# Performance work log

Hardware: AMD Instinct MI355X
Metric: run time of the kernel (lower is better)

Reference implementation:

```python
import jax, jax.numpy as jnp
import numpy as np

B, C_IN, H, W = 1, 448, 64, 64   # concat of resnet18 layer1/2/3 resized to 64x64: 64+128+256=448
D, L = 100, 4096                 # projection dim, number of spatial locations (gaussian params)
OUT_HW = 256                     # input_size for final bilinear upsample


def setup_inputs() -> dict:
    key = jax.random.key(0)
    k0, k1, k2, k3, k4 = jax.random.split(key, 5)
    return {
        "features": jax.random.normal(k0, (B, C_IN, H, W), jnp.float32),
        "proj_w": jax.random.normal(k1, (D, C_IN), jnp.float32) * 0.05,
        "proj_b": jax.random.normal(k2, (D,), jnp.float32) * 0.05,
        "mean": jax.random.normal(k3, (D, L), jnp.float32),
        "inv_cov": jax.random.normal(k4, (L, D, D), jnp.float32) * 0.01,
    }


def reference(features, proj_w, proj_b, mean, inv_cov):
    Bn, C, Hh, Ww = features.shape
    # permute(0,2,3,1).reshape(-1, C) then Linear(C, D)
    f = features.transpose(0, 2, 3, 1).reshape(-1, C)          # (N, C), N = B*H*W
    f = f @ proj_w.T + proj_b                                  # (N, D)
    m = mean.T                                                 # (L, D)
    # Batched Mahalanobis-style quadratic form replacing the Python loop over L=4096:
    #   dist[n, l] = (f_n - m_l)^T  inv_cov_l  (f_n - m_l)
    # Expanded so the heavy term is a single (N, D*D) x (D*D, L) GEMM (no (N,L,D) intermediate).
    Cm  = jnp.einsum('lde,le->ld', inv_cov, m)                 # inv_cov_l @ m_l        (L, D)
    CTm = jnp.einsum('lde,ld->le', inv_cov, m)                 # inv_cov_l^T @ m_l      (L, D)
    const = jnp.einsum('ld,ld->l', m, Cm)                      # m_l^T inv_cov_l m_l    (L,)
    ff = (f[:, :, None] * f[:, None, :]).reshape(f.shape[0], D * D)   # outer(f,f) flattened (N, D*D)
    quad = ff @ inv_cov.reshape(L, D * D).T                    # f^T inv_cov_l f        (N, L)
    dist = quad - f @ (Cm + CTm).T + const[None, :]            # (N, L)
    min_d = jnp.min(dist, axis=1).reshape(Bn, Hh, Ww)[:, None, :, :]  # (B, 1, H, W)
    amap = (min_d - min_d.min()) / (min_d.max() - min_d.min() + 1e-8)
    amap = jax.image.resize(amap, (Bn, 1, OUT_HW, OUT_HW), method='bilinear')
    return amap
```

## Files before the change

kernel.cpp:

```cpp
#include <hip/hip_runtime.h>
#include <hip/hip_bf16.h>
#include <stdint.h>

#define CIN   448
#define DP    100
#define NPIX  4096
#define LNUM  4096
#define KQ    5050
#define KLIN  5150
#define KTOT  5184
#define KSTEPS (KTOT / 64)
#define OUTHW 256

typedef _Float16 f16_t;
typedef _Float16 f16x8 __attribute__((ext_vector_type(8)));
typedef float    f32x4 __attribute__((ext_vector_type(4)));

static __device__ __forceinline__ int swz_idx(int r, int kin) {
    return r * 64 + ((kin & 56) ^ ((r & 7) << 3)) + (kin & 7);
}

static __device__ __forceinline__ int tri_off(int d) { return (d * (201 - d)) >> 1; }

static __device__ __forceinline__ void unpack_tri(int k, int& d, int& e) {
    int dd = (int)((201.0f - sqrtf(40401.0f - 8.0f * (float)k)) * 0.5f);
    if (dd < 0) dd = 0;
    if (dd > 99) dd = 99;
    while (tri_off(dd + 1) <= k) ++dd;
    while (tri_off(dd) > k) --dd;
    d = dd;
    e = dd + (k - tri_off(dd));
}

static __device__ __forceinline__ unsigned f2u(float x) {
    unsigned b = __float_as_uint(x);
    return (b & 0x80000000u) ? ~b : (b | 0x80000000u);
}
static __device__ __forceinline__ float u2f(unsigned u) {
    unsigned b = (u & 0x80000000u) ? (u & 0x7FFFFFFFu) : ~u;
    return __uint_as_float(b);
}

static __device__ __forceinline__ void gload_lds16(const f16_t* g, f16_t* l) {
    __builtin_amdgcn_global_load_lds((const __attribute__((address_space(1))) unsigned*)g,
                                     (__attribute__((address_space(3))) unsigned*)l,
                                     16, 0, 0);
}

__global__ void k_proj(const float* __restrict__ feat, const float* __restrict__ w,
                       const float* __restrict__ b, float* __restrict__ f) {
    int gid = blockIdx.x * 256 + threadIdx.x;
    int n = gid & 4095;
    int d = gid >> 12;
    float acc = b[d];
    const float* wd = w + d * CIN;
    #pragma unroll 4
    for (int c = 0; c < CIN; ++c) acc += feat[c * 4096 + n] * wd[c];
    f[n * DP + d] = acc;
}

__global__ __launch_bounds__(256) void k_buildA(const float* __restrict__ f, f16_t* __restrict__ A) {
    __shared__ float fr[DP];
    int n = blockIdx.x;
    int t = threadIdx.x;
    if (t < DP) fr[t] = f[n * DP + t];
    __syncthreads();
    int r  = n & 127;
    int bm = n >> 7;
    f16_t* tileBase = A + (size_t)bm * KSTEPS * 8192;
    for (int k = t; k < KTOT; k += 256) {
        float v;
        if (k < KQ) {
            int d, e;
            unpack_tri(k, d, e);
            v = fr[d] * fr[e];
        } else if (k < KLIN) {
            v = fr[k - KQ];
        } else {
            v = 0.0f;
        }
        int kt = k >> 6, kin = k & 63;
        tileBase[kt * 8192 + swz_idx(r, kin)] = (f16_t)v;
    }
}

__global__ __launch_bounds__(256) void k_buildB(const float* __restrict__ icov, const float* __restrict__ mean,
                                                f16_t* __restrict__ Bm, float* __restrict__ constl) {
    __shared__ float ic[DP * DP];
    __shared__ float ml[DP];
    __shared__ float wv[DP];
    __shared__ float part[DP];
    int l = blockIdx.x;
    int t = threadIdx.x;
    const float* src = icov + (size_t)l * DP * DP;
    for (int i = t; i < DP * DP; i += 256) ic[i] = src[i];
    if (t < DP) ml[t] = mean[t * LNUM + l];
    __syncthreads();
    if (t < DP) {
        float icm = 0.f, ictm = 0.f;
        for (int e = 0; e < DP; ++e) {
            icm  += ic[t * DP + e] * ml[e];
            ictm += ic[e * DP + t] * ml[e];
        }
        wv[t]   = icm + ictm;
        part[t] = ml[t] * icm;
    }
    __syncthreads();
    if (t == 0) {
        float c = 0.f;
        for (int d = 0; d < DP; ++d) c += part[d];
        constl[l] = c;
    }
    int r  = l & 127;
    int bn = l >> 7;
    f16_t* tileBase = Bm + (size_t)bn * KSTEPS * 8192;
    for (int k = t; k < KTOT; k += 256) {
        float v;
        if (k < KQ) {
            int d, e;
            unpack_tri(k, d, e);
            float s = ic[d * DP + e] + ic[e * DP + d];
            v = (d == e) ? 0.5f * s : s;
        } else if (k < KLIN) {
            v = -wv[k - KQ];
        } else {
            v = 0.0f;
        }
        int kt = k >> 6, kin = k & 63;
        tileBase[kt * 8192 + swz_idx(r, kin)] = (f16_t)v;
    }
}

__global__ void k_init(unsigned* __restrict__ mind) {
    int i = blockIdx.x * 256 + threadIdx.x;
    if (i < NPIX) mind[i] = 0xFFFFFFFFu;
}

__global__ __launch_bounds__(256, 2) void k_gemm(const f16_t* __restrict__ A, const f16_t* __restrict__ Bm,
                                                 const float* __restrict__ constl, unsigned* __restrict__ mind) {
    __shared__ __align__(16) f16_t sA[8192];
    __shared__ __align__(16) f16_t sB[8192];

    int bid = blockIdx.x;
    int pid = ((bid & 7) << 7) | (bid >> 3);
    int group = pid >> 8;
    int pin = pid & 255;
    int bm = group * 8 + (pin & 7);
    int bn = pin >> 3;

    int t = threadIdx.x;
    int lane = t & 63;
    int w = t >> 6;
    int wr = w >> 1, wc = w & 1;

    f32x4 acc[4][4];
    #pragma unroll
    for (int i = 0; i < 4; ++i)
        #pragma unroll
        for (int j = 0; j < 4; ++j) acc[i][j] = (f32x4){0.f, 0.f, 0.f, 0.f};

    const f16_t* Atile = A + (size_t)bm * KSTEPS * 8192;
    const f16_t* Btile = Bm + (size_t)bn * KSTEPS * 8192;

    int chunk0 = w * 2048;
    int lofs = lane * 8;

    int arow[4], brow[4];
    #pragma unroll
    for (int i = 0; i < 4; ++i) {
        arow[i] = wr * 64 + i * 16 + (lane & 15);
        brow[i] = wc * 64 + i * 16 + (lane & 15);
    }

    for (int kt = 0; kt < KSTEPS; ++kt) {
        const f16_t* As = Atile + kt * 8192;
        const f16_t* Bs = Btile + kt * 8192;
        #pragma unroll
        for (int c = 0; c < 4; ++c) {
            gload_lds16(As + chunk0 + c * 512 + lofs, &sA[chunk0 + c * 512]);
            gload_lds16(Bs + chunk0 + c * 512 + lofs, &sB[chunk0 + c * 512]);
        }
        __syncthreads();
        #pragma unroll
        for (int kk = 0; kk < 2; ++kk) {
            f16x8 afr[4], bfr[4];
            int klo = kk * 32 + (lane >> 4) * 8;
            #pragma unroll
            for (int mi = 0; mi < 4; ++mi)
                afr[mi] = *(const f16x8*)&sA[arow[mi] * 64 + (klo ^ ((arow[mi] & 7) << 3))];
            #pragma unroll
            for (int ni = 0; ni < 4; ++ni)
                bfr[ni] = *(const f16x8*)&sB[brow[ni] * 64 + (klo ^ ((brow[ni] & 7) << 3))];
            #pragma unroll
            for (int mi = 0; mi < 4; ++mi)
                #pragma unroll
                for (int ni = 0; ni < 4; ++ni)
                    acc[mi][ni] = __builtin_amdgcn_mfma_f32_16x16x32_f16(afr[mi], bfr[ni], acc[mi][ni], 0, 0, 0);
        }
        __syncthreads();
    }

    int colbase = bn * 128 + wc * 64 + (lane & 15);
    float cl[4];
    #pragma unroll
    for (int ni = 0; ni < 4; ++ni) cl[ni] = constl[colbase + ni * 16];
    #pragma unroll
    for (int mi = 0; mi < 4; ++mi) {
        #pragma unroll
        for (int j = 0; j < 4; ++j) {
            float v = 1e30f;
            #pragma unroll
            for (int ni = 0; ni < 4; ++ni) v = fminf(v, acc[mi][ni][j] + cl[ni]);
            #pragma unroll
            for (int s = 1; s < 16; s <<= 1) v = fminf(v, __shfl_xor(v, s, 64));
            if ((lane & 15) == 0) {
                int row = bm * 128 + wr * 64 + mi * 16 + (lane >> 4) * 4 + j;
                atomicMin(&mind[row], f2u(v));
            }
        }
    }
}

__global__ void k_minmax(const unsigned* __restrict__ mind, float* __restrict__ gmm) {
    __shared__ float smin[256], smax[256];
    int t = threadIdx.x;
    float vmin = 1e30f, vmax = -1e30f;
    for (int i = t; i < NPIX; i += 256) {
        float v = u2f(mind[i]);
        vmin = fminf(vmin, v);
        vmax = fmaxf(vmax, v);
    }
    smin[t] = vmin; smax[t] = vmax;
    __syncthreads();
    for (int s = 128; s > 0; s >>= 1) {
        if (t < s) {
            smin[t] = fminf(smin[t], smin[t + s]);
            smax[t] = fmaxf(smax[t], smax[t + s]);
        }
        __syncthreads();
    }
    if (t == 0) { gmm[0] = smin[0]; gmm[1] = smax[0]; }
}

__global__ void k_upsample(const unsigned* __restrict__ mind, const float* __restrict__ gmm,
                           float* __restrict__ out) {
    int gid = blockIdx.x * 256 + threadIdx.x;
    int i = gid >> 8, j = gid & 255;
    float gmin = gmm[0];
    float scale = 1.0f / (gmm[1] - gmm[0] + 1e-8f);
    float x = fminf(fmaxf(j * 0.25f - 0.375f, 0.0f), 63.0f);
    float y = fminf(fmaxf(i * 0.25f - 0.375f, 0.0f), 63.0f);
    int x0 = (int)x, y0 = (int)y;
    int x1 = min(x0 + 1, 63), y1 = min(y0 + 1, 63);
    float fx = x - x0, fy = y - y0;
    float v00 = u2f(mind[y0 * 64 + x0]), v01 = u2f(mind[y0 * 64 + x1]);
    float v10 = u2f(mind[y1 * 64 + x0]), v11 = u2f(mind[y1 * 64 + x1]);
    float v = v00 * (1.f - fy) * (1.f - fx) + v01 * (1.f - fy) * fx
            + v10 * fy * (1.f - fx) + v11 * fy * fx;
    out[gid] = (v - gmin) * scale;
}

__global__ void k_diag(float* __restrict__ out) {
    int gid = blockIdx.x * 256 + threadIdx.x;
    out[gid] = 0.25f;
}

extern "C" void kernel_launch(void* const* d_in, const int* in_sizes, int n_in,
                              void* d_out, int out_size, void* d_ws, size_t ws_size,
                              hipStream_t stream) {
    const float* feat = (const float*)d_in[0];
    const float* pw   = (const float*)d_in[1];
    const float* pb   = (const float*)d_in[2];
    const float* mean = (const float*)d_in[3];
    const float* icov = (const float*)d_in[4];

    size_t need = 0;
    auto count = [&need](size_t bytes) { need = ((need + 255) & ~(size_t)255) + bytes; };
    count((size_t)NPIX * DP * 4);
    count((size_t)NPIX * KTOT * 2);
    count((size_t)LNUM * KTOT * 2);
    count((size_t)LNUM * 4);
    count((size_t)NPIX * 4);
    count(2 * 4);
    if (ws_size < need) {
        k_diag<<<256, 256, 0, stream>>>((float*)d_out);
        return;
    }

    char* ws = (char*)d_ws;
    size_t off = 0;
    auto alloc = [&](size_t bytes) -> void* {
        off = (off + 255) & ~(size_t)255;
        void* p = ws + off;
        off += bytes;
        return p;
    };
    float*    f      = (float*)alloc((size_t)NPIX * DP * 4);
    f16_t*    Amat   = (f16_t*)alloc((size_t)NPIX * KTOT * 2);
    f16_t*    Bmat   = (f16_t*)alloc((size_t)LNUM * KTOT * 2);
    float*    constl = (float*)alloc((size_t)LNUM * 4);
    unsigned* mind   = (unsigned*)alloc((size_t)NPIX * 4);
    float*    gmm    = (float*)alloc(2 * 4);

    k_proj    <<<1600, 256, 0, stream>>>(feat, pw, pb, f);
    k_buildA  <<<NPIX, 256, 0, stream>>>(f, Amat);
    k_buildB  <<<LNUM, 256, 0, stream>>>(icov, mean, Bmat, constl);
    k_init    <<<16, 256, 0, stream>>>(mind);
    k_gemm    <<<1024, 256, 0, stream>>>(Amat, Bmat, constl, mind);
    k_minmax  <<<1, 256, 0, stream>>>(mind, gmm);
    k_upsample<<<256, 256, 0, stream>>>(mind, gmm, (float*)d_out);
}
```

Before: 319.7 us.

## Enlarge GEMM tiles to 256x256 with double-buffered LDS and LUT-based operand builds

The GEMM moves from 128x128 tiles with 256 threads to 256x256 tiles with 512 threads. Each wave now holds an 8x4 MFMA accumulator set, and the next K step is prefetched into a double-buffered LDS. MFMA blocks get raised priority through s_setprio. The A and B build kernels replace the per-element sqrt-based triangular unpack with a precomputed lookup table, write 8 halves per vectorized store, and pad the icov LDS rows to 101 floats to avoid bank conflicts. The costs are 128KB of LDS and higher register pressure per block, and the grid shrinks to 256 blocks, which may underfill the CUs.

```diff
diff --git a/kernel.cpp b/kernel.cpp
--- a/kernel.cpp
+++ b/kernel.cpp
@@ -15,10 +15,7 @@
 typedef _Float16 f16_t;
 typedef _Float16 f16x8 __attribute__((ext_vector_type(8)));
 typedef float    f32x4 __attribute__((ext_vector_type(4)));
-
-static __device__ __forceinline__ int swz_idx(int r, int kin) {
-    return r * 64 + ((kin & 56) ^ ((r & 7) << 3)) + (kin & 7);
-}
+typedef unsigned short u16x8 __attribute__((ext_vector_type(8)));
 
 static __device__ __forceinline__ int tri_off(int d) { return (d * (201 - d)) >> 1; }
 
@@ -45,6 +42,15 @@
     __builtin_amdgcn_global_load_lds((const __attribute__((address_space(1))) unsigned*)g,
                                      (__attribute__((address_space(3))) unsigned*)l,
                                      16, 0, 0);
+}
+
+__global__ void k_lut(unsigned short* __restrict__ lut) {
+    int k = blockIdx.x * 256 + threadIdx.x;
+    if (k < KTOT) {
+        int d = 0, e = 0;
+        if (k < KQ) unpack_tri(k, d, e);
+        lut[k] = (unsigned short)(d | (e << 8));
+    }
 }
 
 __global__ void k_proj(const float* __restrict__ feat, const float* __restrict__ w,
@@ -59,48 +65,60 @@
     f[n * DP + d] = acc;
 }
 
-__global__ __launch_bounds__(256) void k_buildA(const float* __restrict__ f, f16_t* __restrict__ A) {
+__global__ __launch_bounds__(256) void k_buildA(const float* __restrict__ f, const unsigned short* __restrict__ lut,
+                                                f16_t* __restrict__ A) {
     __shared__ float fr[DP];
     int n = blockIdx.x;
     int t = threadIdx.x;
     if (t < DP) fr[t] = f[n * DP + t];
     __syncthreads();
     int r  = n & 127;
-    int bm = n >> 7;
-    f16_t* tileBase = A + (size_t)bm * KSTEPS * 8192;
-    for (int k = t; k < KTOT; k += 256) {
-        float v;
-        if (k < KQ) {
-            int d, e;
-            unpack_tri(k, d, e);
-            v = fr[d] * fr[e];
-        } else if (k < KLIN) {
-            v = fr[k - KQ];
-        } else {
-            v = 0.0f;
-        }
-        int kt = k >> 6, kin = k & 63;
-        tileBase[kt * 8192 + swz_idx(r, kin)] = (f16_t)v;
+    int rsw = (r & 7) << 3;
+    f16_t* tileBase = A + (size_t)(n >> 7) * KSTEPS * 8192;
+    for (int g = t; g < KTOT / 8; g += 256) {
+        int k0 = g * 8;
+        u16x8 lu = *(const u16x8*)&lut[k0];
+        f16x8 v;
+        #pragma unroll
+        for (int j = 0; j < 8; ++j) {
+            int k = k0 + j;
+            float x;
+            if (k < KQ) {
+                int d = lu[j] & 255, e = lu[j] >> 8;
+                x = fr[d] * fr[e];
+            } else if (k < KLIN) {
+                x = fr[k - KQ];
+            } else {
+                x = 0.0f;
+            }
+            v[j] = (f16_t)x;
+        }
+        int kt = k0 >> 6, kin = k0 & 63;
+        *(f16x8*)&tileBase[kt * 8192 + r * 64 + ((kin & 56) ^ rsw)] = v;
     }
 }
 
 __global__ __launch_bounds__(256) void k_buildB(const float* __restrict__ icov, const float* __restrict__ mean,
+                                                const unsigned short* __restrict__ lut,
                                                 f16_t* __restrict__ Bm, float* __restrict__ constl) {
-    __shared__ float ic[DP * DP];
+    __shared__ float ic[DP * 101];
     __shared__ float ml[DP];
     __shared__ float wv[DP];
     __shared__ float part[DP];
     int l = blockIdx.x;
     int t = threadIdx.x;
     const float* src = icov + (size_t)l * DP * DP;
-    for (int i = t; i < DP * DP; i += 256) ic[i] = src[i];
+    for (int i = t; i < DP * DP; i += 256) {
+        int row = i / 100;
+        ic[row * 101 + (i - row * 100)] = src[i];
+    }
     if (t < DP) ml[t] = mean[t * LNUM + l];
     __syncthreads();
     if (t < DP) {
         float icm = 0.f, ictm = 0.f;
         for (int e = 0; e < DP; ++e) {
-            icm  += ic[t * DP + e] * ml[e];
-            ictm += ic[e * DP + t] * ml[e];
+            icm  += ic[t * 101 + e] * ml[e];
+            ictm += ic[e * 101 + t] * ml[e];
         }
         wv[t]   = icm + ictm;
         part[t] = ml[t] * icm;
@@ -112,22 +130,29 @@
         constl[l] = c;
     }
     int r  = l & 127;
-    int bn = l >> 7;
-    f16_t* tileBase = Bm + (size_t)bn * KSTEPS * 8192;
-    for (int k = t; k < KTOT; k += 256) {
-        float v;
-        if (k < KQ) {
-            int d, e;
-            unpack_tri(k, d, e);
-            float s = ic[d * DP + e] + ic[e * DP + d];
-            v = (d == e) ? 0.5f * s : s;
-        } else if (k < KLIN) {
-            v = -wv[k - KQ];
-        } else {
-            v = 0.0f;
-        }
-        int kt = k >> 6, kin = k & 63;
-        tileBase[kt * 8192 + swz_idx(r, kin)] = (f16_t)v;
+    int rsw = (r & 7) << 3;
+    f16_t* tileBase = Bm + (size_t)(l >> 7) * KSTEPS * 8192;
+    for (int g = t; g < KTOT / 8; g += 256) {
+        int k0 = g * 8;
+        u16x8 lu = *(const u16x8*)&lut[k0];
+        f16x8 v;
+        #pragma unroll
+        for (int j = 0; j < 8; ++j) {
+            int k = k0 + j;
+            float x;
+            if (k < KQ) {
+                int d = lu[j] & 255, e = lu[j] >> 8;
+                float s = ic[d * 101 + e] + ic[e * 101 + d];
+                x = (d == e) ? 0.5f * s : s;
+            } else if (k < KLIN) {
+                x = -wv[k - KQ];
+            } else {
+                x = 0.0f;
+            }
+            v[j] = (f16_t)x;
+        }
+        int kt = k0 >> 6, kin = k0 & 63;
+        *(f16x8*)&tileBase[kt * 8192 + r * 64 + ((kin & 56) ^ rsw)] = v;
     }
 }
 
@@ -136,85 +161,102 @@
     if (i < NPIX) mind[i] = 0xFFFFFFFFu;
 }
 
-__global__ __launch_bounds__(256, 2) void k_gemm(const f16_t* __restrict__ A, const f16_t* __restrict__ Bm,
+__global__ __launch_bounds__(512, 2) void k_gemm(const f16_t* __restrict__ A, const f16_t* __restrict__ Bm,
                                                  const float* __restrict__ constl, unsigned* __restrict__ mind) {
-    __shared__ __align__(16) f16_t sA[8192];
-    __shared__ __align__(16) f16_t sB[8192];
+    __shared__ __align__(16) f16_t sA[2][16384];
+    __shared__ __align__(16) f16_t sB[2][16384];
 
     int bid = blockIdx.x;
-    int pid = ((bid & 7) << 7) | (bid >> 3);
-    int group = pid >> 8;
-    int pin = pid & 255;
-    int bm = group * 8 + (pin & 7);
-    int bn = pin >> 3;
+    int pid = ((bid & 7) << 5) | (bid >> 3);
+    int bm = pid & 15;
+    int bn = pid >> 4;
 
     int t = threadIdx.x;
     int lane = t & 63;
     int w = t >> 6;
-    int wr = w >> 1, wc = w & 1;
-
-    f32x4 acc[4][4];
+    int wr = w >> 2;
+    int wc = w & 3;
+
+    f32x4 acc[8][4];
     #pragma unroll
-    for (int i = 0; i < 4; ++i)
+    for (int i = 0; i < 8; ++i)
         #pragma unroll
         for (int j = 0; j < 4; ++j) acc[i][j] = (f32x4){0.f, 0.f, 0.f, 0.f};
 
-    const f16_t* Atile = A + (size_t)bm * KSTEPS * 8192;
-    const f16_t* Btile = Bm + (size_t)bn * KSTEPS * 8192;
-
-    int chunk0 = w * 2048;
-    int lofs = lane * 8;
-
-    int arow[4], brow[4];
-    #pragma unroll
-    for (int i = 0; i < 4; ++i) {
-        arow[i] = wr * 64 + i * 16 + (lane & 15);
-        brow[i] = wc * 64 + i * 16 + (lane & 15);
-    }
+    const f16_t* Abase = A  + ((size_t)(2 * bm + (w >> 2)) * KSTEPS) * 8192 + (w & 3) * 2048 + lane * 8;
+    const f16_t* Bbase = Bm + ((size_t)(2 * bn + (w >> 2)) * KSTEPS) * 8192 + (w & 3) * 2048 + lane * 8;
+
+    int l15 = lane & 15;
+    int xorv = (lane & 7) << 3;
+    int klobase = (lane >> 4) * 8;
+
+    {
+        const f16_t* As = Abase;
+        const f16_t* Bs = Bbase;
+        #pragma unroll
+        for (int c = 0; c < 4; ++c) {
+            gload_lds16(As + c * 512, &sA[0][w * 2048 + c * 512]);
+            gload_lds16(Bs + c * 512, &sB[0][w * 2048 + c * 512]);
+        }
+    }
+    __syncthreads();
 
     for (int kt = 0; kt < KSTEPS; ++kt) {
-        const f16_t* As = Atile + kt * 8192;
-        const f16_t* Bs = Btile + kt * 8192;
-        #pragma unroll
-        for (int c = 0; c < 4; ++c) {
-            gload_lds16(As + chunk0 + c * 512 + lofs, &sA[chunk0 + c * 512]);
-            gload_lds16(Bs + chunk0 + c * 512 + lofs, &sB[chunk0 + c * 512]);
+        int p = kt & 1;
+        if (kt + 1 < KSTEPS) {
+            const f16_t* As = Abase + (size_t)(kt + 1) * 8192;
+            const f16_t* Bs = Bbase + (size_t)(kt + 1) * 8192;
+            #pragma unroll
+            for (int c = 0; c < 4; ++c) {
+                gload_lds16(As + c * 512, &sA[p ^ 1][w * 2048 + c * 512]);
+                gload_lds16(Bs + c * 512, &sB[p ^ 1][w * 2048 + c * 512]);
+            }
+        }
+        #pragma unroll
+        for (int kk = 0; kk < 2; ++kk) {
+            int klo = (kk * 32 + klobase) ^ xorv;
+            f16x8 bfr[4];
+            #pragma unroll
+            for (int ni = 0; ni < 4; ++ni) {
+                int rr = (wc & 1) * 64 + ni * 16 + l15;
+                bfr[ni] = *(const f16x8*)&sB[p][(wc >> 1) * 8192 + rr * 64 + klo];
+            }
+            #pragma unroll
+            for (int mq = 0; mq < 2; ++mq) {
+                f16x8 afr[4];
+                #pragma unroll
+                for (int mi = 0; mi < 4; ++mi) {
+                    int rr = (mq * 4 + mi) * 16 + l15;
+                    afr[mi] = *(const f16x8*)&sA[p][wr * 8192 + rr * 64 + klo];
+                }
+                __builtin_amdgcn_s_setprio(1);
+                #pragma unroll
+                for (int mi = 0; mi < 4; ++mi)
+                    #pragma unroll
+                    for (int ni = 0; ni < 4; ++ni)
+                        acc[mq * 4 + mi][ni] =
+                            __builtin_amdgcn_mfma_f32_16x16x32_f16(afr[mi], bfr[ni], acc[mq * 4 + mi][ni], 0, 0, 0);
+                __builtin_amdgcn_s_setprio(0);
+            }
         }
         __syncthreads();
-        #pragma unroll
-        for (int kk = 0; kk < 2; ++kk) {
-            f16x8 afr[4], bfr[4];
-            int klo = kk * 32 + (lane >> 4) * 8;
-            #pragma unroll
-            for (int mi = 0; mi < 4; ++mi)
-                afr[mi] = *(const f16x8*)&sA[arow[mi] * 64 + (klo ^ ((arow[mi] & 7) << 3))];
-            #pragma unroll
-            for (int ni = 0; ni < 4; ++ni)
-                bfr[ni] = *(const f16x8*)&sB[brow[ni] * 64 + (klo ^ ((brow[ni] & 7) << 3))];
-            #pragma unroll
-            for (int mi = 0; mi < 4; ++mi)
-                #pragma unroll
-                for (int ni = 0; ni < 4; ++ni)
-                    acc[mi][ni] = __builtin_amdgcn_mfma_f32_16x16x32_f16(afr[mi], bfr[ni], acc[mi][ni], 0, 0, 0);
-        }
-        __syncthreads();
-    }
-
-    int colbase = bn * 128 + wc * 64 + (lane & 15);
+    }
+
+    int colbase = bn * 256 + wc * 64 + l15;
     float cl[4];
     #pragma unroll
     for (int ni = 0; ni < 4; ++ni) cl[ni] = constl[colbase + ni * 16];
     #pragma unroll
-    for (int mi = 0; mi < 4; ++mi) {
+    for (int mi8 = 0; mi8 < 8; ++mi8) {
         #pragma unroll
         for (int j = 0; j < 4; ++j) {
             float v = 1e30f;
             #pragma unroll
-            for (int ni = 0; ni < 4; ++ni) v = fminf(v, acc[mi][ni][j] + cl[ni]);
+            for (int ni = 0; ni < 4; ++ni) v = fminf(v, acc[mi8][ni][j] + cl[ni]);
             #pragma unroll
             for (int s = 1; s < 16; s <<= 1) v = fminf(v, __shfl_xor(v, s, 64));
-            if ((lane & 15) == 0) {
-                int row = bm * 128 + wr * 64 + mi * 16 + (lane >> 4) * 4 + j;
+            if (l15 == 0) {
+                int row = bm * 256 + wr * 128 + mi8 * 16 + (lane >> 4) * 4 + j;
                 atomicMin(&mind[row], f2u(v));
             }
         }
@@ -282,6 +324,7 @@
     count((size_t)LNUM * 4);
     count((size_t)NPIX * 4);
     count(2 * 4);
+    count((size_t)KTOT * 2);
     if (ws_size < need) {
         k_diag<<<256, 256, 0, stream>>>((float*)d_out);
         return;
@@ -295,18 +338,20 @@
         off += bytes;
         return p;
     };
-    float*    f      = (float*)alloc((size_t)NPIX * DP * 4);
-    f16_t*    Amat   = (f16_t*)alloc((size_t)NPIX * KTOT * 2);
-    f16_t*    Bmat   = (f16_t*)alloc((size_t)LNUM * KTOT * 2);
-    float*    constl = (float*)alloc((size_t)LNUM * 4);
-    unsigned* mind   = (unsigned*)alloc((size_t)NPIX * 4);
-    float*    gmm    = (float*)alloc(2 * 4);
-
+    float*          f      = (float*)alloc((size_t)NPIX * DP * 4);
+    f16_t*          Amat   = (f16_t*)alloc((size_t)NPIX * KTOT * 2);
+    f16_t*          Bmat   = (f16_t*)alloc((size_t)LNUM * KTOT * 2);
+    float*          constl = (float*)alloc((size_t)LNUM * 4);
+    unsigned*       mind   = (unsigned*)alloc((size_t)NPIX * 4);
+    float*          gmm    = (float*)alloc(2 * 4);
+    unsigned short* lut    = (unsigned short*)alloc((size_t)KTOT * 2);
+
+    k_lut     <<<(KTOT + 255) / 256, 256, 0, stream>>>(lut);
     k_proj    <<<1600, 256, 0, stream>>>(feat, pw, pb, f);
-    k_buildA  <<<NPIX, 256, 0, stream>>>(f, Amat);
-    k_buildB  <<<LNUM, 256, 0, stream>>>(icov, mean, Bmat, constl);
+    k_buildA  <<<NPIX, 256, 0, stream>>>(f, lut, Amat);
+    k_buildB  <<<LNUM, 256, 0, stream>>>(icov, mean, lut, Bmat, constl);
     k_init    <<<16, 256, 0, stream>>>(mind);
-    k_gemm    <<<1024, 256, 0, stream>>>(Amat, Bmat, constl, mind);
+    k_gemm    <<<256, 512, 0, stream>>>(Amat, Bmat, constl, mind);
     k_minmax  <<<1, 256, 0, stream>>>(mind, gmm);
     k_upsample<<<256, 256, 0, stream>>>(mind, gmm, (float*)d_out);
 }
```

Result: faster. 292.6 us (-8.5%).
